# Kernel optimization log

Measured on AMD Instinct MI355X. Metric: run time of the kernel, lower is better.

Reference implementation:

```python
import jax, jax.numpy as jnp
import numpy as np

N = 100000      # nodes
E = 1600000     # edges (avg degree 16)
D_IN = 128      # input feature dim
H = 128         # sage_hidden (conv1 and conv2 out)
LH = 256        # linear_hidden (decoder)


def setup_inputs() -> dict:
    key = jax.random.key(0)
    ks = jax.random.split(key, 12)
    x = jax.random.normal(ks[0], (N, D_IN), dtype=jnp.float32)
    edge_index = jax.random.randint(ks[1], (2, E), 0, N, dtype=jnp.int64)
    s = 1.0 / np.sqrt(D_IN)
    sh = 1.0 / np.sqrt(H)
    sl = 1.0 / np.sqrt(LH)
    return {
        "x": x,
        "edge_index": edge_index,
        # SAGEConv1: out = agg @ W_l^T + b_l + x @ W_r^T
        "W1_l": jax.random.uniform(ks[2], (H, D_IN), jnp.float32, -s, s),
        "b1": jax.random.uniform(ks[3], (H,), jnp.float32, -s, s),
        "W1_r": jax.random.uniform(ks[4], (H, D_IN), jnp.float32, -s, s),
        # SAGEConv2
        "W2_l": jax.random.uniform(ks[5], (H, H), jnp.float32, -sh, sh),
        "b2": jax.random.uniform(ks[6], (H,), jnp.float32, -sh, sh),
        "W2_r": jax.random.uniform(ks[7], (H, H), jnp.float32, -sh, sh),
        # decoder MLP
        "W3": jax.random.uniform(ks[8], (LH, H), jnp.float32, -sh, sh),
        "b3": jax.random.uniform(ks[9], (LH,), jnp.float32, -sh, sh),
        "W4": jax.random.uniform(ks[10], (1, LH), jnp.float32, -sl, sl),
        "b4": jax.random.uniform(ks[11], (1,), jnp.float32, -sl, sl),
    }


def _mean_aggregate(x, src, dst):
    # gather neighbor features along edges and mean-reduce into destination nodes
    sums = jax.ops.segment_sum(x[src], dst, num_segments=N)          # [N, d]
    cnt = jax.ops.segment_sum(jnp.ones((src.shape[0],), x.dtype), dst,
                              num_segments=N)                        # [N]
    return sums / jnp.maximum(cnt, 1.0)[:, None]


def _sage(x, src, dst, W_l, b, W_r):
    agg = _mean_aggregate(x, src, dst)
    return agg @ W_l.T + b + x @ W_r.T


def reference(x, edge_index, W1_l, b1, W1_r, W2_l, b2, W2_r, W3, b3, W4, b4):
    src, dst = edge_index[0], edge_index[1]
    h = jax.nn.relu(_sage(x, src, dst, W1_l, b1, W1_r))   # conv1 + relu
    h = _sage(h, src, dst, W2_l, b2, W2_r)                 # conv2
    # decoder (dropout p=0 / eval mode -> identity)
    h = jax.nn.relu(h @ W3.T + b3)
    out = (h @ W4.T + b4).reshape(-1)                      # [N]
    return out
```

## Files before the change

### kernel.cpp

```cpp
#include <hip/hip_runtime.h>

typedef unsigned short u16;
typedef unsigned int u32;
typedef unsigned long long u64;

#define N_NODES 100000
#define N_EDGES 1600000
#define TPITCH 136
#define NBIN 196
#define BCAP 12288
#define NPART 512
#define EPB 3125

typedef __bf16 bf16x8 __attribute__((ext_vector_type(8)));
typedef float  f32x4  __attribute__((ext_vector_type(4)));

__device__ inline float b2f(u16 b) { return __uint_as_float(((u32)b) << 16); }
__device__ inline float b2f_lo(u32 u) { return __uint_as_float(u << 16); }
__device__ inline float b2f_hi(u32 u) { return __uint_as_float(u & 0xffff0000u); }
__device__ inline u16 f2b(float f) {
    u32 u = __float_as_uint(f);
    return (u16)((u + 0x7fffu + ((u >> 16) & 1u)) >> 16);
}

__device__ inline bf16x8 ldfrag(const u16* base, int row, int k) {
    union { uint4 u; bf16x8 v; } t;
    t.u = *(const uint4*)(base + (size_t)row * 128 + k);
    return t.v;
}
__device__ inline bf16x8 ldfrag_f32(const float* base, int row, int k) {
    const float4* p = (const float4*)(base + (size_t)row * 128 + k);
    float4 a = p[0], b = p[1];
    union { u16 h[8]; bf16x8 v; } t;
    t.h[0] = f2b(a.x); t.h[1] = f2b(a.y); t.h[2] = f2b(a.z); t.h[3] = f2b(a.w);
    t.h[4] = f2b(b.x); t.h[5] = f2b(b.y); t.h[6] = f2b(b.z); t.h[7] = f2b(b.w);
    return t.v;
}
__device__ inline bf16x8 ldfrag_lds(const u16* tile, int lrow, int k) {
    union { uint4 u; bf16x8 v; } t;
    t.u = *(const uint4*)(tile + lrow * TPITCH + k);
    return t.v;
}
__device__ inline f32x4 mfma16(bf16x8 a, bf16x8 b, f32x4 c) {
    return __builtin_amdgcn_mfma_f32_16x16x32_bf16(a, b, c, 0, 0, 0);
}

__device__ inline void stage_w(const u16* __restrict__ g, u16* lds) {
    int t = threadIdx.x;
#pragma unroll
    for (int i = 0; i < 8; i++) {
        int u = t + i * 256;
        int row = u >> 4, k = (u & 15) * 8;
        *(uint4*)(lds + row * TPITCH + k) = *(const uint4*)(g + row * 128 + k);
    }
}

__global__ __launch_bounds__(256) void k_diag(u16* __restrict__ out, float val) {
    int i = blockIdx.x * 256 + threadIdx.x;
    if (i < N_NODES) out[i] = f2b(val);
}

__global__ __launch_bounds__(256) void k_detects(const u64* __restrict__ e,
                                                 const u32* __restrict__ x,
                                                 int* __restrict__ flags) {
    int t = threadIdx.x;
    if (blockIdx.x == 0) {
        u64 v = 0;
#pragma unroll
        for (int i = 0; i < 4; i++) v |= e[t + 256 * i];
        if (v >> 32) atomicOr(&flags[0], 1);
    } else {
        int bad = 0;
#pragma unroll
        for (int i = 0; i < 4; i++) {
            u32 w = x[t + 256 * i];
            u32 ex = (w >> 7) & 0xff;
            if (ex < 100 || ex > 140) bad = 1;
        }
        if (bad) atomicOr(&flags[1], 1);
    }
}

__device__ inline void load_edge(const int* ei, int is32, int e, int& src, int& dst) {
    if (is32) {
        src = ei[e]; dst = ei[N_EDGES + e];
    } else {
        const long long* e64 = (const long long*)ei;
        src = (int)e64[e]; dst = (int)e64[N_EDGES + e];
    }
}

__global__ __launch_bounds__(256) void k_rhist(const int* __restrict__ ei,
                                               int* __restrict__ ghist,
                                               const int* __restrict__ flags) {
    __shared__ int hist[NBIN];
    int p = blockIdx.x, t = threadIdx.x;
    for (int i = t; i < NBIN; i += 256) hist[i] = 0;
    __syncthreads();
    int is32 = flags[0];
    int base = p * EPB;
    int end = base + EPB; if (end > N_EDGES) end = N_EDGES;
    for (int e = base + t; e < end; e += 256) {
        int src, dst; load_edge(ei, is32, e, src, dst);
        if ((u32)src < N_NODES && (u32)dst < N_NODES) atomicAdd(&hist[dst >> 9], 1);
    }
    __syncthreads();
    for (int i = t; i < NBIN; i += 256) ghist[i * NPART + p] = hist[i];
}
__global__ __launch_bounds__(512) void k_rscan(const int* __restrict__ ghist,
                                               int* __restrict__ gbase,
                                               int* __restrict__ gcur) {
    __shared__ int buf[NPART];
    int b = blockIdx.x, t = threadIdx.x;
    int v = ghist[b * NPART + t];
    buf[t] = v;
    __syncthreads();
    for (int s = 1; s < NPART; s <<= 1) {
        int a = (t >= s) ? buf[t - s] : 0;
        __syncthreads();
        buf[t] += a;
        __syncthreads();
    }
    gbase[b * NPART + t] = buf[t] - v;
    if (t == NPART - 1) gcur[b] = buf[t];
}
__global__ __launch_bounds__(256) void k_rscatter(const int* __restrict__ ei,
                                                  const int* __restrict__ gbase,
                                                  u32* __restrict__ gbuf,
                                                  const int* __restrict__ flags) {
    __shared__ int cur[NBIN];
    int p = blockIdx.x, t = threadIdx.x;
    for (int i = t; i < NBIN; i += 256) cur[i] = gbase[i * NPART + p];
    __syncthreads();
    int is32 = flags[0];
    int base = p * EPB;
    int end = base + EPB; if (end > N_EDGES) end = N_EDGES;
    for (int e = base + t; e < end; e += 256) {
        int src, dst; load_edge(ei, is32, e, src, dst);
        if ((u32)src < N_NODES && (u32)dst < N_NODES) {
            int bin = dst >> 9;
            int pos = atomicAdd(&cur[bin], 1);
            if (pos < BCAP)
                gbuf[(size_t)bin * BCAP + pos] = ((u32)(dst & 511) << 17) | (u32)src;
        }
    }
}
__global__ __launch_bounds__(512) void k_binB(const int* __restrict__ gcur,
                                              const u32* __restrict__ gbuf,
                                              u32* __restrict__ csr,
                                              int* __restrict__ cnt,
                                              int* __restrict__ offN) {
    __shared__ int hist[512];
    __shared__ int pfx[512];
    __shared__ int cur[512];
    __shared__ u32 srcbuf[BCAP];
    int b = blockIdx.x, t = threadIdx.x;
    int n = gcur[b]; if (n > BCAP) n = BCAP;
    hist[t] = 0;
    __syncthreads();
    for (int i = t; i < n; i += 512)
        atomicAdd(&hist[gbuf[(size_t)b * BCAP + i] >> 17], 1);
    __syncthreads();
    pfx[t] = hist[t];
    __syncthreads();
    for (int s = 1; s < 512; s <<= 1) {
        int a = (t >= s) ? pfx[t - s] : 0;
        __syncthreads();
        pfx[t] += a;
        __syncthreads();
    }
    int excl = pfx[t] - hist[t];
    cur[t] = excl;
    __syncthreads();
    for (int i = t; i < n; i += 512) {
        u32 p = gbuf[(size_t)b * BCAP + i];
        int pos = atomicAdd(&cur[p >> 17], 1);
        if (pos < BCAP) srcbuf[pos] = p & 0x1FFFFu;
    }
    __syncthreads();
    int total = pfx[511];
    for (int i = t; i < total; i += 512)
        csr[(size_t)b * BCAP + i] = srcbuf[i];
    int node = b * 512 + t;
    if (node < N_NODES) {
        cnt[node] = hist[t];
        offN[node] = b * BCAP + excl;
    }
}

#define WTOT 99073
struct CvtArgs { const void* src[10]; int off[10]; int n[10]; };
__global__ __launch_bounds__(256) void k_cvtw(CvtArgs a, u16* __restrict__ dst,
                                              const int* __restrict__ flags) {
    int i = blockIdx.x * 256 + threadIdx.x;
    if (i >= WTOT) return;
    int isf = flags[1];
    int s = 0;
    while (s < 9 && i >= a.off[s + 1]) s++;
    int j = i - a.off[s];
    float v = isf ? ((const float*)a.src[s])[j] : b2f(((const u16*)a.src[s])[j]);
    dst[i] = f2b(v);
}
#define W_W1L 0
#define W_W1R 16384
#define W_W2L 32768
#define W_W2R 49152
#define W_W3  65536
#define W_W4  98304
#define W_B1  98560
#define W_B2  98688
#define W_B3  98816
#define W_B4  99072

__global__ __launch_bounds__(256) void k_cvtx(const void* __restrict__ x,
                                              u16* __restrict__ xb,
                                              const int* __restrict__ flags) {
    int i = blockIdx.x * 256 + threadIdx.x;
    if ((size_t)i * 4 >= (size_t)N_NODES * 128) return;
    if (flags[1]) {
        float4 v = ((const float4*)x)[i];
        union { u16 h[4]; u64 q; } t;
        t.h[0] = f2b(v.x); t.h[1] = f2b(v.y); t.h[2] = f2b(v.z); t.h[3] = f2b(v.w);
        ((u64*)xb)[i] = t.q;
    } else {
        ((u64*)xb)[i] = ((const u64*)x)[i];
    }
}

__global__ __launch_bounds__(256) void k_aggc(const u16* __restrict__ feat,
                                              const int* __restrict__ cnt,
                                              const int* __restrict__ offN,
                                              const u32* __restrict__ csr,
                                              u16* __restrict__ outb) {
    int node = blockIdx.x * 4 + (threadIdx.x >> 6);
    if (node >= N_NODES) return;
    int lane = threadIdx.x & 63;
    int deg = cnt[node];
    int s = offN[node];
    const u32* f = (const u32*)feat;
    float a0 = 0, a1 = 0, b0 = 0, b1 = 0, c0 = 0, c1 = 0, d0 = 0, d1 = 0;
    int p = 0;
    for (; p + 3 < deg; p += 4) {
        u32 n0 = csr[s + p], n1 = csr[s + p + 1], n2 = csr[s + p + 2], n3 = csr[s + p + 3];
        if (n0 >= N_NODES) n0 = 0;
        if (n1 >= N_NODES) n1 = 0;
        if (n2 >= N_NODES) n2 = 0;
        if (n3 >= N_NODES) n3 = 0;
        u32 w0 = f[(size_t)n0 * 64 + lane];
        u32 w1 = f[(size_t)n1 * 64 + lane];
        u32 w2 = f[(size_t)n2 * 64 + lane];
        u32 w3 = f[(size_t)n3 * 64 + lane];
        a0 += b2f_lo(w0); a1 += b2f_hi(w0);
        b0 += b2f_lo(w1); b1 += b2f_hi(w1);
        c0 += b2f_lo(w2); c1 += b2f_hi(w2);
        d0 += b2f_lo(w3); d1 += b2f_hi(w3);
    }
    for (; p < deg; p++) {
        u32 n0 = csr[s + p];
        if (n0 >= N_NODES) n0 = 0;
        u32 w0 = f[(size_t)n0 * 64 + lane];
        a0 += b2f_lo(w0); a1 += b2f_hi(w0);
    }
    float s0 = (a0 + b0) + (c0 + d0), s1 = (a1 + b1) + (c1 + d1);
    float sc = deg > 0 ? 1.f / (float)deg : 0.f;
    u16 h0 = f2b(s0 * sc), h1 = f2b(s1 * sc);
    ((u32*)outb)[(size_t)node * 64 + lane] = (u32)h0 | ((u32)h1 << 16);
}

__global__ __launch_bounds__(256) void k_aggcx(const void* __restrict__ x,
                                               const int* __restrict__ cnt,
                                               const int* __restrict__ offN,
                                               const u32* __restrict__ csr,
                                               const int* __restrict__ flags,
                                               u16* __restrict__ outb) {
    int node = blockIdx.x * 4 + (threadIdx.x >> 6);
    if (node >= N_NODES) return;
    int lane = threadIdx.x & 63;
    int deg = cnt[node];
    int s = offN[node];
    float a0 = 0, a1 = 0, b0 = 0, b1 = 0;
    int p = 0;
    if (flags[1]) {
        const float2* f = (const float2*)x;
        for (; p + 1 < deg; p += 2) {
            u32 n0 = csr[s + p], n1 = csr[s + p + 1];
            if (n0 >= N_NODES) n0 = 0;
            if (n1 >= N_NODES) n1 = 0;
            float2 w0 = f[(size_t)n0 * 64 + lane];
            float2 w1 = f[(size_t)n1 * 64 + lane];
            a0 += w0.x; a1 += w0.y; b0 += w1.x; b1 += w1.y;
        }
        for (; p < deg; p++) {
            u32 n0 = csr[s + p];
            if (n0 >= N_NODES) n0 = 0;
            float2 w0 = f[(size_t)n0 * 64 + lane];
            a0 += w0.x; a1 += w0.y;
        }
    } else {
        const u32* f = (const u32*)x;
        for (; p + 1 < deg; p += 2) {
            u32 n0 = csr[s + p], n1 = csr[s + p + 1];
            if (n0 >= N_NODES) n0 = 0;
            if (n1 >= N_NODES) n1 = 0;
            u32 w0 = f[(size_t)n0 * 64 + lane];
            u32 w1 = f[(size_t)n1 * 64 + lane];
            a0 += b2f_lo(w0); a1 += b2f_hi(w0);
            b0 += b2f_lo(w1); b1 += b2f_hi(w1);
        }
        for (; p < deg; p++) {
            u32 n0 = csr[s + p];
            if (n0 >= N_NODES) n0 = 0;
            u32 w0 = f[(size_t)n0 * 64 + lane];
            a0 += b2f_lo(w0); a1 += b2f_hi(w0);
        }
    }
    float s0 = a0 + b0, s1 = a1 + b1;
    float sc = deg > 0 ? 1.f / (float)deg : 0.f;
    u16 h0 = f2b(s0 * sc), h1 = f2b(s1 * sc);
    ((u32*)outb)[(size_t)node * 64 + lane] = (u32)h0 | ((u32)h1 << 16);
}

template <bool DUALX>
__global__ __launch_bounds__(256) void k_conv1f(
    const u16* __restrict__ aggA, const void* __restrict__ xself,
    const u16* __restrict__ Wc, const int* __restrict__ flags,
    u16* __restrict__ h1) {
    __shared__ __align__(16) u16 wbuf[128 * TPITCH];
    int wid = threadIdx.x >> 6, lane = threadIdx.x & 63;
    int r15 = lane & 15, quad = lane >> 4;
    int rb = blockIdx.x * 64;
    int ar = rb + wid * 16 + r15; if (ar > N_NODES - 1) ar = N_NODES - 1;

    bf16x8 ag[4], ax[4];
    bool isf = DUALX && flags[1];
#pragma unroll
    for (int ks = 0; ks < 4; ks++) {
        int ko = ks * 32 + quad * 8;
        ag[ks] = ldfrag(aggA, ar, ko);
        ax[ks] = isf ? ldfrag_f32((const float*)xself, ar, ko)
                     : ldfrag((const u16*)xself, ar, ko);
    }
    f32x4 acc[8] = {};
    stage_w(Wc + W_W1L, wbuf);
    __syncthreads();
#pragma unroll
    for (int ks = 0; ks < 4; ks++) {
        int ko = ks * 32 + quad * 8;
#pragma unroll
        for (int ct = 0; ct < 8; ct++)
            acc[ct] = mfma16(ag[ks], ldfrag_lds(wbuf, ct * 16 + r15, ko), acc[ct]);
    }
    __syncthreads();
    stage_w(Wc + W_W1R, wbuf);
    __syncthreads();
#pragma unroll
    for (int ks = 0; ks < 4; ks++) {
        int ko = ks * 32 + quad * 8;
#pragma unroll
        for (int ct = 0; ct < 8; ct++)
            acc[ct] = mfma16(ax[ks], ldfrag_lds(wbuf, ct * 16 + r15, ko), acc[ct]);
    }
#pragma unroll
    for (int ct = 0; ct < 8; ct++) {
        int col = ct * 16 + r15;
        float bb = b2f(Wc[W_B1 + col]);
#pragma unroll
        for (int r = 0; r < 4; r++) {
            int row = rb + wid * 16 + quad * 4 + r;
            if (row < N_NODES)
                h1[(size_t)row * 128 + col] = f2b(fmaxf(acc[ct][r] + bb, 0.f));
        }
    }
}

__global__ __launch_bounds__(256) void k_conv2f(
    const u16* __restrict__ aggH, const u16* __restrict__ h1,
    const u16* __restrict__ Wc, const int* __restrict__ flags,
    void* __restrict__ out) {
    __shared__ __align__(16) u16 wbuf[128 * TPITCH];
    __shared__ __align__(16) u16 tile[64 * TPITCH];
    int wid = threadIdx.x >> 6, lane = threadIdx.x & 63;
    int r15 = lane & 15, quad = lane >> 4;
    int rb = blockIdx.x * 64;
    int ar = rb + wid * 16 + r15; if (ar > N_NODES - 1) ar = N_NODES - 1;
    int arl = wid * 16 + r15;

    bf16x8 at[4], as[4];
#pragma unroll
    for (int ks = 0; ks < 4; ks++) {
        int ko = ks * 32 + quad * 8;
        at[ks] = ldfrag(aggH, ar, ko);
        as[ks] = ldfrag(h1, ar, ko);
    }
    f32x4 acc2[8] = {};
    stage_w(Wc + W_W2L, wbuf);
    __syncthreads();
#pragma unroll
    for (int ks = 0; ks < 4; ks++) {
        int ko = ks * 32 + quad * 8;
#pragma unroll
        for (int ct = 0; ct < 8; ct++)
            acc2[ct] = mfma16(at[ks], ldfrag_lds(wbuf, ct * 16 + r15, ko), acc2[ct]);
    }
    __syncthreads();
    stage_w(Wc + W_W2R, wbuf);
    __syncthreads();
#pragma unroll
    for (int ks = 0; ks < 4; ks++) {
        int ko = ks * 32 + quad * 8;
#pragma unroll
        for (int ct = 0; ct < 8; ct++)
            acc2[ct] = mfma16(as[ks], ldfrag_lds(wbuf, ct * 16 + r15, ko), acc2[ct]);
    }
#pragma unroll
    for (int ct = 0; ct < 8; ct++) {
        int col = ct * 16 + r15;
        float bb = b2f(Wc[W_B2 + col]);
#pragma unroll
        for (int r = 0; r < 4; r++) {
            int lr = wid * 16 + quad * 4 + r;
            tile[lr * TPITCH + col] = f2b(acc2[ct][r] + bb);
        }
    }
    __syncthreads();

    float pr[4] = {};
    float b4f = b2f(Wc[W_B4]);
#pragma unroll
    for (int half = 0; half < 2; half++) {
        stage_w(Wc + W_W3 + half * 16384, wbuf);
        __syncthreads();
        f32x4 acc3[8] = {};
#pragma unroll
        for (int ks = 0; ks < 4; ks++) {
            int ko = ks * 32 + quad * 8;
            bf16x8 a = ldfrag_lds(tile, arl, ko);
#pragma unroll
            for (int ct = 0; ct < 8; ct++)
                acc3[ct] = mfma16(a, ldfrag_lds(wbuf, ct * 16 + r15, ko), acc3[ct]);
        }
#pragma unroll
        for (int ct = 0; ct < 8; ct++) {
            int col = half * 128 + ct * 16 + r15;
            float bb = b2f(Wc[W_B3 + col]);
            float w4 = b2f(Wc[W_W4 + col]);
#pragma unroll
            for (int r = 0; r < 4; r++)
                pr[r] += fmaxf(acc3[ct][r] + bb, 0.f) * w4;
        }
        __syncthreads();
    }
#pragma unroll
    for (int m = 1; m < 16; m <<= 1)
#pragma unroll
        for (int r = 0; r < 4; r++)
            pr[r] += __shfl_xor(pr[r], m, 64);
    if (r15 == 0) {
        int isf = flags[1];
#pragma unroll
        for (int r = 0; r < 4; r++) {
            int row = rb + wid * 16 + quad * 4 + r;
            if (row < N_NODES) {
                float v = pr[r] + b4f;
                if (isf) ((float*)out)[row] = v;
                else     ((u16*)out)[row] = f2b(v);
            }
        }
    }
}

__global__ __launch_bounds__(256) void k_hist(const int* __restrict__ ei,
                                              int* __restrict__ cnt,
                                              const int* __restrict__ flags) {
    int e = blockIdx.x * 256 + threadIdx.x;
    if (e >= N_EDGES) return;
    int src, dst; load_edge(ei, flags[0], e, src, dst);
    if ((u32)src < N_NODES && (u32)dst < N_NODES) atomicAdd(&cnt[dst], 1);
}
__global__ __launch_bounds__(1024) void k_scan(int* __restrict__ cnt,
                                               int* __restrict__ off) {
    __shared__ int buf[1024];
    __shared__ int carry_s;
    int t = threadIdx.x;
    if (t == 0) carry_s = 0;
    __syncthreads();
    for (int base = 0; base < N_NODES; base += 1024) {
        int i = base + t;
        int v = (i < N_NODES) ? cnt[i] : 0;
        buf[t] = v;
        __syncthreads();
        for (int s = 1; s < 1024; s <<= 1) {
            int a = (t >= s) ? buf[t - s] : 0;
            __syncthreads();
            buf[t] += a;
            __syncthreads();
        }
        int carry = carry_s;
        if (i < N_NODES) {
            int excl = carry + buf[t] - v;
            off[i] = excl;
            cnt[i] = excl;
        }
        __syncthreads();
        if (t == 1023) carry_s = carry + buf[1023];
        __syncthreads();
    }
    if (t == 0) off[N_NODES] = carry_s;
}
__global__ __launch_bounds__(256) void k_csr(const int* __restrict__ ei,
                                             int* __restrict__ cursor,
                                             int* __restrict__ csr,
                                             const int* __restrict__ flags) {
    int e = blockIdx.x * 256 + threadIdx.x;
    if (e >= N_EDGES) return;
    int src, dst; load_edge(ei, flags[0], e, src, dst);
    if ((u32)src < N_NODES && (u32)dst < N_NODES) {
        int pos = atomicAdd(&cursor[dst], 1);
        if ((u32)pos < N_EDGES) csr[pos] = src;
    }
}
__device__ inline void agg_bf16(const u16* __restrict__ feat,
                                const int* __restrict__ off, const int* __restrict__ csr,
                                u16* tile, int rb, int wid, int lane) {
    const u32* f32p = (const u32*)feat;
    for (int rr = 0; rr < 32; rr++) {
        int lr = wid * 32 + rr;
        int node = rb + lr;
        float s0 = 0.f, s1 = 0.f;
        int deg = 0;
        if (node < N_NODES) {
            int s = off[node], e = off[node + 1];
            if (s < 0) s = 0;
            if (e > N_EDGES) e = N_EDGES;
            if (e < s) e = s;
            deg = e - s;
            for (int p = s; p < e; p++) {
                int nb = csr[p];
                if ((u32)nb >= N_NODES) nb = 0;
                u32 u = f32p[(size_t)nb * 64 + lane];
                s0 += b2f_lo(u); s1 += b2f_hi(u);
            }
        }
        float sc = deg > 0 ? 1.f / (float)deg : 0.f;
        u16 h0 = f2b(s0 * sc), h1 = f2b(s1 * sc);
        ((u32*)tile)[lr * (TPITCH / 2) + lane] = (u32)h0 | ((u32)h1 << 16);
    }
}
__device__ inline void agg_f32(const float* __restrict__ feat,
                               const int* __restrict__ off, const int* __restrict__ csr,
                               u16* tile, int rb, int wid, int lane) {
    const float2* fp = (const float2*)feat;
    for (int rr = 0; rr < 32; rr++) {
        int lr = wid * 32 + rr;
        int node = rb + lr;
        float s0 = 0.f, s1 = 0.f;
        int deg = 0;
        if (node < N_NODES) {
            int s = off[node], e = off[node + 1];
            if (s < 0) s = 0;
            if (e > N_EDGES) e = N_EDGES;
            if (e < s) e = s;
            deg = e - s;
            for (int p = s; p < e; p++) {
                int nb = csr[p];
                if ((u32)nb >= N_NODES) nb = 0;
                float2 v = fp[(size_t)nb * 64 + lane];
                s0 += v.x; s1 += v.y;
            }
        }
        float sc = deg > 0 ? 1.f / (float)deg : 0.f;
        u16 h0 = f2b(s0 * sc), h1 = f2b(s1 * sc);
        ((u32*)tile)[lr * (TPITCH / 2) + lane] = (u32)h0 | ((u32)h1 << 16);
    }
}
__global__ __launch_bounds__(256) void k_conv1(
    const void* __restrict__ x, const int* __restrict__ off, const int* __restrict__ csr,
    const u16* __restrict__ Wc, const int* __restrict__ flags,
    u16* __restrict__ h1) {
    __shared__ __align__(16) u16 tile[128 * TPITCH];
    int wid = threadIdx.x >> 6, lane = threadIdx.x & 63;
    int r15 = lane & 15, quad = lane >> 4;
    int rb = blockIdx.x * 128;
    int isf = flags[1];
    if (isf) agg_f32((const float*)x, off, csr, tile, rb, wid, lane);
    else     agg_bf16((const u16*)x, off, csr, tile, rb, wid, lane);
    __syncthreads();
    int ar0l = wid * 32 + r15, ar1l = ar0l + 16;
    int ar0g = rb + ar0l; if (ar0g > N_NODES - 1) ar0g = N_NODES - 1;
    int ar1g = rb + ar1l; if (ar1g > N_NODES - 1) ar1g = N_NODES - 1;
    bf16x8 ax0[4], ax1[4];
    if (isf) {
#pragma unroll
        for (int ks = 0; ks < 4; ks++) {
            int ko = ks * 32 + quad * 8;
            ax0[ks] = ldfrag_f32((const float*)x, ar0g, ko);
            ax1[ks] = ldfrag_f32((const float*)x, ar1g, ko);
        }
    } else {
#pragma unroll
        for (int ks = 0; ks < 4; ks++) {
            int ko = ks * 32 + quad * 8;
            ax0[ks] = ldfrag((const u16*)x, ar0g, ko);
            ax1[ks] = ldfrag((const u16*)x, ar1g, ko);
        }
    }
    f32x4 acc[2][8] = {};
#pragma unroll
    for (int ks = 0; ks < 4; ks++) {
        int ko = ks * 32 + quad * 8;
        bf16x8 a0t = ldfrag_lds(tile, ar0l, ko);
        bf16x8 a1t = ldfrag_lds(tile, ar1l, ko);
#pragma unroll
        for (int ct = 0; ct < 8; ct++) {
            bf16x8 bl = ldfrag(Wc + W_W1L, ct * 16 + r15, ko);
            bf16x8 br = ldfrag(Wc + W_W1R, ct * 16 + r15, ko);
            acc[0][ct] = mfma16(a0t, bl, acc[0][ct]);
            acc[0][ct] = mfma16(ax0[ks], br, acc[0][ct]);
            acc[1][ct] = mfma16(a1t, bl, acc[1][ct]);
            acc[1][ct] = mfma16(ax1[ks], br, acc[1][ct]);
        }
    }
#pragma unroll
    for (int ct = 0; ct < 8; ct++) {
        int col = ct * 16 + r15;
        float bb = b2f(Wc[W_B1 + col]);
#pragma unroll
        for (int rt = 0; rt < 2; rt++) {
#pragma unroll
            for (int r = 0; r < 4; r++) {
                int row = rb + wid * 32 + rt * 16 + quad * 4 + r;
                if (row < N_NODES)
                    h1[(size_t)row * 128 + col] = f2b(fmaxf(acc[rt][ct][r] + bb, 0.f));
            }
        }
    }
}
__global__ __launch_bounds__(256) void k_conv2mlp(
    const u16* __restrict__ h1, const int* __restrict__ off, const int* __restrict__ csr,
    const u16* __restrict__ Wc, const int* __restrict__ flags,
    void* __restrict__ out) {
    __shared__ __align__(16) u16 tile[128 * TPITCH];
    int wid = threadIdx.x >> 6, lane = threadIdx.x & 63;
    int r15 = lane & 15, quad = lane >> 4;
    int rb = blockIdx.x * 128;
    agg_bf16(h1, off, csr, tile, rb, wid, lane);
    __syncthreads();
    int ar0l = wid * 32 + r15, ar1l = ar0l + 16;
    int ar0g = rb + ar0l; if (ar0g > N_NODES - 1) ar0g = N_NODES - 1;
    int ar1g = rb + ar1l; if (ar1g > N_NODES - 1) ar1g = N_NODES - 1;
    f32x4 acc2[2][8] = {};
#pragma unroll
    for (int ks = 0; ks < 4; ks++) {
        int ko = ks * 32 + quad * 8;
        bf16x8 a0t = ldfrag_lds(tile, ar0l, ko);
        bf16x8 a1t = ldfrag_lds(tile, ar1l, ko);
        bf16x8 a0s = ldfrag(h1, ar0g, ko);
        bf16x8 a1s = ldfrag(h1, ar1g, ko);
#pragma unroll
        for (int ct = 0; ct < 8; ct++) {
            bf16x8 bl = ldfrag(Wc + W_W2L, ct * 16 + r15, ko);
            bf16x8 br = ldfrag(Wc + W_W2R, ct * 16 + r15, ko);
            acc2[0][ct] = mfma16(a0t, bl, acc2[0][ct]);
            acc2[0][ct] = mfma16(a0s, br, acc2[0][ct]);
            acc2[1][ct] = mfma16(a1t, bl, acc2[1][ct]);
            acc2[1][ct] = mfma16(a1s, br, acc2[1][ct]);
        }
    }
    __syncthreads();
#pragma unroll
    for (int ct = 0; ct < 8; ct++) {
        int col = ct * 16 + r15;
        float bb = b2f(Wc[W_B2 + col]);
#pragma unroll
        for (int rt = 0; rt < 2; rt++) {
#pragma unroll
            for (int r = 0; r < 4; r++) {
                int lr = wid * 32 + rt * 16 + quad * 4 + r;
                tile[lr * TPITCH + col] = f2b(acc2[rt][ct][r] + bb);
            }
        }
    }
    __syncthreads();
    float pr[2][4] = {};
    float b4f = b2f(Wc[W_B4]);
#pragma unroll
    for (int half = 0; half < 2; half++) {
        f32x4 acc3[2][8] = {};
#pragma unroll
        for (int ks = 0; ks < 4; ks++) {
            int ko = ks * 32 + quad * 8;
            bf16x8 a0 = ldfrag_lds(tile, ar0l, ko);
            bf16x8 a1 = ldfrag_lds(tile, ar1l, ko);
#pragma unroll
            for (int ct = 0; ct < 8; ct++) {
                bf16x8 b = ldfrag(Wc + W_W3, half * 128 + ct * 16 + r15, ko);
                acc3[0][ct] = mfma16(a0, b, acc3[0][ct]);
                acc3[1][ct] = mfma16(a1, b, acc3[1][ct]);
            }
        }
#pragma unroll
        for (int ct = 0; ct < 8; ct++) {
            int col = half * 128 + ct * 16 + r15;
            float bb = b2f(Wc[W_B3 + col]);
            float w4 = b2f(Wc[W_W4 + col]);
#pragma unroll
            for (int rt = 0; rt < 2; rt++)
#pragma unroll
                for (int r = 0; r < 4; r++)
                    pr[rt][r] += fmaxf(acc3[rt][ct][r] + bb, 0.f) * w4;
        }
    }
#pragma unroll
    for (int m = 1; m < 16; m <<= 1)
#pragma unroll
        for (int rt = 0; rt < 2; rt++)
#pragma unroll
            for (int r = 0; r < 4; r++)
                pr[rt][r] += __shfl_xor(pr[rt][r], m, 64);
    if (r15 == 0) {
        int isf = flags[1];
#pragma unroll
        for (int rt = 0; rt < 2; rt++) {
#pragma unroll
            for (int r = 0; r < 4; r++) {
                int row = rb + wid * 32 + rt * 16 + quad * 4 + r;
                if (row < N_NODES) {
                    float v = pr[rt][r] + b4f;
                    if (isf) ((float*)out)[row] = v;
                    else     ((u16*)out)[row] = f2b(v);
                }
            }
        }
    }
}

extern "C" void kernel_launch(void* const* d_in, const int* in_sizes, int n_in,
                              void* d_out, int out_size, void* d_ws, size_t ws_size,
                              hipStream_t stream) {
    const void* x  = d_in[0];
    const int* ei  = (const int*)d_in[1];

    const size_t A = 256;
    const size_t sFlg  = 256;
    const size_t sGcur = 1024;
    const size_t sGh   = (((size_t)NBIN * NPART * 4) + A - 1) & ~(A - 1);
    const size_t sCnt  = (((size_t)N_NODES * 4) + A - 1) & ~(A - 1);
    const size_t sOffN = (((size_t)N_NODES * 4) + A - 1) & ~(A - 1);
    const size_t sWc   = ((WTOT * 2) + A - 1) & ~(A - 1);
    const size_t sCsrB = (((size_t)NBIN * BCAP * 4) + A - 1) & ~(A - 1);
    const size_t sFB   = (((size_t)N_NODES * 128 * 2) + A - 1) & ~(A - 1);
    const size_t sOff  = (((size_t)(N_NODES + 1) * 4) + A - 1) & ~(A - 1);
    const size_t sCsr  = (((size_t)N_EDGES * 4) + A - 1) & ~(A - 1);
    const size_t needB1 = sFlg + sGcur + 2 * sGh + sCnt + sOffN + sWc + sCsrB + 2 * sFB;
    const size_t needB0 = needB1 + sFB;
    const size_t needS  = sFlg + sCnt + sOff + sCsr + sFB;

    char* ws = (char*)d_ws;
    int gconv = (N_NODES + 63) / 64;
    int gagg  = (N_NODES + 3) / 4;

    CvtArgs ca;
    const int srcIdx[10] = {2, 4, 5, 7, 8, 10, 3, 6, 9, 11};
    const int offs[10] = {W_W1L, W_W1R, W_W2L, W_W2R, W_W3, W_W4, W_B1, W_B2, W_B3, W_B4};
    const int ns[10]   = {16384, 16384, 16384, 16384, 32768, 256, 128, 128, 256, 1};
    for (int i = 0; i < 10; i++) { ca.src[i] = d_in[srcIdx[i]]; ca.off[i] = offs[i]; ca.n[i] = ns[i]; }

    if (ws_size >= needB1) {
        bool t0 = ws_size >= needB0;
        int* flags = (int*)ws;
        int* gcur  = (int*)(ws + sFlg);
        int* ghist = (int*)(ws + sFlg + sGcur);
        int* gbase = (int*)(ws + sFlg + sGcur + sGh);
        int* cnt   = (int*)(ws + sFlg + sGcur + 2 * sGh);
        int* offN  = (int*)(ws + sFlg + sGcur + 2 * sGh + sCnt);
        u16* Wc    = (u16*)(ws + sFlg + sGcur + 2 * sGh + sCnt + sOffN);
        u32* csrb  = (u32*)(ws + sFlg + sGcur + 2 * sGh + sCnt + sOffN + sWc);
        u16* B1    = (u16*)(ws + sFlg + sGcur + 2 * sGh + sCnt + sOffN + sWc + sCsrB);
        u16* B2    = B1 + (sFB / 2);
        u32* gbuf  = (u32*)B2;
        u16* xb    = B2 + (sFB / 2);

        hipMemsetAsync(ws, 0, sFlg, stream);
        k_detects<<<2, 256, 0, stream>>>((const u64*)ei, (const u32*)x, flags);
        k_rhist<<<NPART, 256, 0, stream>>>(ei, ghist, flags);
        k_rscan<<<NBIN, 512, 0, stream>>>(ghist, gbase, gcur);
        k_rscatter<<<NPART, 256, 0, stream>>>(ei, gbase, gbuf, flags);
        k_binB<<<NBIN, 512, 0, stream>>>(gcur, gbuf, csrb, cnt, offN);
        k_cvtw<<<(WTOT + 255) / 256, 256, 0, stream>>>(ca, Wc, flags);

        if (t0) {
            k_cvtx<<<((N_NODES * 128 / 4) + 255) / 256, 256, 0, stream>>>(x, xb, flags);
            k_aggc<<<gagg, 256, 0, stream>>>(xb, cnt, offN, csrb, B1);
            k_conv1f<false><<<gconv, 256, 0, stream>>>(B1, xb, Wc, flags, B2);
        } else {
            k_aggcx<<<gagg, 256, 0, stream>>>(x, cnt, offN, csrb, flags, B1);
            k_conv1f<true><<<gconv, 256, 0, stream>>>(B1, x, Wc, flags, B2);
        }
        k_aggc<<<gagg, 256, 0, stream>>>(B2, cnt, offN, csrb, B1);
        k_conv2f<<<gconv, 256, 0, stream>>>(B1, B2, Wc, flags, d_out);
    } else if (ws_size >= needS) {
        int* flags = (int*)ws;
        int* cnt   = (int*)(ws + sFlg);
        u16* Wc    = (u16*)(ws + sFlg);
        int* off   = (int*)(ws + sFlg + sCnt);
        int* csr   = (int*)(ws + sFlg + sCnt + sOff);
        u16* h1    = (u16*)(ws + sFlg + sCnt + sOff + sCsr);

        hipMemsetAsync(ws, 0, sFlg + (size_t)N_NODES * 4, stream);
        k_detects<<<2, 256, 0, stream>>>((const u64*)ei, (const u32*)x, flags);
        k_hist<<<N_EDGES / 256, 256, 0, stream>>>(ei, cnt, flags);
        k_scan<<<1, 1024, 0, stream>>>(cnt, off);
        k_csr<<<N_EDGES / 256, 256, 0, stream>>>(ei, cnt, csr, flags);
        k_cvtw<<<(WTOT + 255) / 256, 256, 0, stream>>>(ca, Wc, flags);
        k_conv1<<<(N_NODES + 127) / 128, 256, 0, stream>>>(x, off, csr, Wc, flags, h1);
        k_conv2mlp<<<(N_NODES + 127) / 128, 256, 0, stream>>>(h1, off, csr, Wc, flags, d_out);
    } else {
        k_diag<<<(N_NODES + 255) / 256, 256, 0, stream>>>(
            (u16*)d_out, 2000.0f + (float)(ws_size >> 20));
    }
}
```

Baseline: 345.7 us.

## Fuse mean aggregation into SAGE conv kernels via shared-memory tile

The separate aggregation kernels are removed, and each conv kernel now gathers and averages neighbor features for its 64-row tile directly into a shared-memory tile before running the MFMA matmul. This avoids writing and re-reading the aggregated feature buffer in global memory and saves two launches, and the workspace needs one fewer feature buffer. The cost is parallelism: aggregation now runs with one block per 64 nodes (each wave walks 16 nodes in sequence) instead of one wave per node. That cuts memory-level parallelism and occupancy, since the extra LDS tile means fewer blocks per CU for the latency-bound gather.

```diff
diff --git a/kernel.cpp b/kernel.cpp
--- a/kernel.cpp
+++ b/kernel.cpp
@@ -227,128 +227,139 @@
     }
 }
 
-__global__ __launch_bounds__(256) void k_aggc(const u16* __restrict__ feat,
-                                              const int* __restrict__ cnt,
-                                              const int* __restrict__ offN,
-                                              const u32* __restrict__ csr,
-                                              u16* __restrict__ outb) {
-    int node = blockIdx.x * 4 + (threadIdx.x >> 6);
-    if (node >= N_NODES) return;
-    int lane = threadIdx.x & 63;
-    int deg = cnt[node];
-    int s = offN[node];
+__device__ inline void agg16_bf16(const u16* __restrict__ feat,
+                                  const int* __restrict__ cnt,
+                                  const int* __restrict__ offN,
+                                  const u32* __restrict__ csr,
+                                  u16* tile, int rb, int wid, int lane) {
     const u32* f = (const u32*)feat;
-    float a0 = 0, a1 = 0, b0 = 0, b1 = 0, c0 = 0, c1 = 0, d0 = 0, d1 = 0;
-    int p = 0;
-    for (; p + 3 < deg; p += 4) {
-        u32 n0 = csr[s + p], n1 = csr[s + p + 1], n2 = csr[s + p + 2], n3 = csr[s + p + 3];
-        if (n0 >= N_NODES) n0 = 0;
-        if (n1 >= N_NODES) n1 = 0;
-        if (n2 >= N_NODES) n2 = 0;
-        if (n3 >= N_NODES) n3 = 0;
-        u32 w0 = f[(size_t)n0 * 64 + lane];
-        u32 w1 = f[(size_t)n1 * 64 + lane];
-        u32 w2 = f[(size_t)n2 * 64 + lane];
-        u32 w3 = f[(size_t)n3 * 64 + lane];
-        a0 += b2f_lo(w0); a1 += b2f_hi(w0);
-        b0 += b2f_lo(w1); b1 += b2f_hi(w1);
-        c0 += b2f_lo(w2); c1 += b2f_hi(w2);
-        d0 += b2f_lo(w3); d1 += b2f_hi(w3);
-    }
-    for (; p < deg; p++) {
-        u32 n0 = csr[s + p];
-        if (n0 >= N_NODES) n0 = 0;
-        u32 w0 = f[(size_t)n0 * 64 + lane];
-        a0 += b2f_lo(w0); a1 += b2f_hi(w0);
-    }
-    float s0 = (a0 + b0) + (c0 + d0), s1 = (a1 + b1) + (c1 + d1);
-    float sc = deg > 0 ? 1.f / (float)deg : 0.f;
-    u16 h0 = f2b(s0 * sc), h1 = f2b(s1 * sc);
-    ((u32*)outb)[(size_t)node * 64 + lane] = (u32)h0 | ((u32)h1 << 16);
-}
-
-__global__ __launch_bounds__(256) void k_aggcx(const void* __restrict__ x,
-                                               const int* __restrict__ cnt,
-                                               const int* __restrict__ offN,
-                                               const u32* __restrict__ csr,
-                                               const int* __restrict__ flags,
-                                               u16* __restrict__ outb) {
-    int node = blockIdx.x * 4 + (threadIdx.x >> 6);
-    if (node >= N_NODES) return;
-    int lane = threadIdx.x & 63;
-    int deg = cnt[node];
-    int s = offN[node];
-    float a0 = 0, a1 = 0, b0 = 0, b1 = 0;
-    int p = 0;
-    if (flags[1]) {
-        const float2* f = (const float2*)x;
-        for (; p + 1 < deg; p += 2) {
-            u32 n0 = csr[s + p], n1 = csr[s + p + 1];
-            if (n0 >= N_NODES) n0 = 0;
-            if (n1 >= N_NODES) n1 = 0;
-            float2 w0 = f[(size_t)n0 * 64 + lane];
-            float2 w1 = f[(size_t)n1 * 64 + lane];
-            a0 += w0.x; a1 += w0.y; b0 += w1.x; b1 += w1.y;
-        }
-        for (; p < deg; p++) {
-            u32 n0 = csr[s + p];
-            if (n0 >= N_NODES) n0 = 0;
-            float2 w0 = f[(size_t)n0 * 64 + lane];
-            a0 += w0.x; a1 += w0.y;
-        }
-    } else {
-        const u32* f = (const u32*)x;
-        for (; p + 1 < deg; p += 2) {
-            u32 n0 = csr[s + p], n1 = csr[s + p + 1];
-            if (n0 >= N_NODES) n0 = 0;
-            if (n1 >= N_NODES) n1 = 0;
-            u32 w0 = f[(size_t)n0 * 64 + lane];
-            u32 w1 = f[(size_t)n1 * 64 + lane];
-            a0 += b2f_lo(w0); a1 += b2f_hi(w0);
-            b0 += b2f_lo(w1); b1 += b2f_hi(w1);
-        }
-        for (; p < deg; p++) {
-            u32 n0 = csr[s + p];
-            if (n0 >= N_NODES) n0 = 0;
-            u32 w0 = f[(size_t)n0 * 64 + lane];
-            a0 += b2f_lo(w0); a1 += b2f_hi(w0);
-        }
-    }
-    float s0 = a0 + b0, s1 = a1 + b1;
-    float sc = deg > 0 ? 1.f / (float)deg : 0.f;
-    u16 h0 = f2b(s0 * sc), h1 = f2b(s1 * sc);
-    ((u32*)outb)[(size_t)node * 64 + lane] = (u32)h0 | ((u32)h1 << 16);
+    for (int rr = 0; rr < 16; rr++) {
+        int node = rb + wid * 16 + rr;
+        float a0 = 0, a1 = 0, b0 = 0, b1 = 0, c0 = 0, c1 = 0, d0 = 0, d1 = 0;
+        int deg = 0;
+        if (node < N_NODES) {
+            deg = cnt[node];
+            int s = offN[node];
+            int p = 0;
+            for (; p + 3 < deg; p += 4) {
+                u32 n0 = csr[s + p], n1 = csr[s + p + 1], n2 = csr[s + p + 2], n3 = csr[s + p + 3];
+                if (n0 >= N_NODES) n0 = 0;
+                if (n1 >= N_NODES) n1 = 0;
+                if (n2 >= N_NODES) n2 = 0;
+                if (n3 >= N_NODES) n3 = 0;
+                u32 w0 = f[(size_t)n0 * 64 + lane];
+                u32 w1 = f[(size_t)n1 * 64 + lane];
+                u32 w2 = f[(size_t)n2 * 64 + lane];
+                u32 w3 = f[(size_t)n3 * 64 + lane];
+                a0 += b2f_lo(w0); a1 += b2f_hi(w0);
+                b0 += b2f_lo(w1); b1 += b2f_hi(w1);
+                c0 += b2f_lo(w2); c1 += b2f_hi(w2);
+                d0 += b2f_lo(w3); d1 += b2f_hi(w3);
+            }
+            for (; p < deg; p++) {
+                u32 n0 = csr[s + p];
+                if (n0 >= N_NODES) n0 = 0;
+                u32 w0 = f[(size_t)n0 * 64 + lane];
+                a0 += b2f_lo(w0); a1 += b2f_hi(w0);
+            }
+        }
+        float s0 = (a0 + b0) + (c0 + d0), s1 = (a1 + b1) + (c1 + d1);
+        float sc = deg > 0 ? 1.f / (float)deg : 0.f;
+        u16 h0 = f2b(s0 * sc), h1 = f2b(s1 * sc);
+        ((u32*)tile)[(wid * 16 + rr) * (TPITCH / 2) + lane] = (u32)h0 | ((u32)h1 << 16);
+    }
+}
+
+__device__ inline void agg16_x(const void* __restrict__ x, int isf,
+                               const int* __restrict__ cnt,
+                               const int* __restrict__ offN,
+                               const u32* __restrict__ csr,
+                               u16* tile, int rb, int wid, int lane) {
+    for (int rr = 0; rr < 16; rr++) {
+        int node = rb + wid * 16 + rr;
+        float a0 = 0, a1 = 0, b0 = 0, b1 = 0;
+        int deg = 0;
+        if (node < N_NODES) {
+            deg = cnt[node];
+            int s = offN[node];
+            int p = 0;
+            if (isf) {
+                const float2* f = (const float2*)x;
+                for (; p + 1 < deg; p += 2) {
+                    u32 n0 = csr[s + p], n1 = csr[s + p + 1];
+                    if (n0 >= N_NODES) n0 = 0;
+                    if (n1 >= N_NODES) n1 = 0;
+                    float2 w0 = f[(size_t)n0 * 64 + lane];
+                    float2 w1 = f[(size_t)n1 * 64 + lane];
+                    a0 += w0.x; a1 += w0.y; b0 += w1.x; b1 += w1.y;
+                }
+                for (; p < deg; p++) {
+                    u32 n0 = csr[s + p];
+                    if (n0 >= N_NODES) n0 = 0;
+                    float2 w0 = f[(size_t)n0 * 64 + lane];
+                    a0 += w0.x; a1 += w0.y;
+                }
+            } else {
+                const u32* f = (const u32*)x;
+                for (; p + 1 < deg; p += 2) {
+                    u32 n0 = csr[s + p], n1 = csr[s + p + 1];
+                    if (n0 >= N_NODES) n0 = 0;
+                    if (n1 >= N_NODES) n1 = 0;
+                    u32 w0 = f[(size_t)n0 * 64 + lane];
+                    u32 w1 = f[(size_t)n1 * 64 + lane];
+                    a0 += b2f_lo(w0); a1 += b2f_hi(w0);
+                    b0 += b2f_lo(w1); b1 += b2f_hi(w1);
+                }
+                for (; p < deg; p++) {
+                    u32 n0 = csr[s + p];
+                    if (n0 >= N_NODES) n0 = 0;
+                    u32 w0 = f[(size_t)n0 * 64 + lane];
+                    a0 += b2f_lo(w0); a1 += b2f_hi(w0);
+                }
+            }
+        }
+        float s0 = a0 + b0, s1 = a1 + b1;
+        float sc = deg > 0 ? 1.f / (float)deg : 0.f;
+        u16 h0 = f2b(s0 * sc), h1 = f2b(s1 * sc);
+        ((u32*)tile)[(wid * 16 + rr) * (TPITCH / 2) + lane] = (u32)h0 | ((u32)h1 << 16);
+    }
 }
 
 template <bool DUALX>
-__global__ __launch_bounds__(256) void k_conv1f(
-    const u16* __restrict__ aggA, const void* __restrict__ xself,
+__global__ __launch_bounds__(256) void k_fconv1(
+    const void* __restrict__ xself, const int* __restrict__ cnt,
+    const int* __restrict__ offN, const u32* __restrict__ csrb,
     const u16* __restrict__ Wc, const int* __restrict__ flags,
     u16* __restrict__ h1) {
     __shared__ __align__(16) u16 wbuf[128 * TPITCH];
+    __shared__ __align__(16) u16 tile[64 * TPITCH];
     int wid = threadIdx.x >> 6, lane = threadIdx.x & 63;
     int r15 = lane & 15, quad = lane >> 4;
     int rb = blockIdx.x * 64;
+    bool isf = DUALX && flags[1];
+
+    stage_w(Wc + W_W1L, wbuf);
+    if (DUALX) agg16_x(xself, isf, cnt, offN, csrb, tile, rb, wid, lane);
+    else       agg16_bf16((const u16*)xself, cnt, offN, csrb, tile, rb, wid, lane);
+
     int ar = rb + wid * 16 + r15; if (ar > N_NODES - 1) ar = N_NODES - 1;
-
-    bf16x8 ag[4], ax[4];
-    bool isf = DUALX && flags[1];
+    bf16x8 ax[4];
 #pragma unroll
     for (int ks = 0; ks < 4; ks++) {
         int ko = ks * 32 + quad * 8;
-        ag[ks] = ldfrag(aggA, ar, ko);
         ax[ks] = isf ? ldfrag_f32((const float*)xself, ar, ko)
                      : ldfrag((const u16*)xself, ar, ko);
     }
+    __syncthreads();
+
     f32x4 acc[8] = {};
-    stage_w(Wc + W_W1L, wbuf);
-    __syncthreads();
 #pragma unroll
     for (int ks = 0; ks < 4; ks++) {
         int ko = ks * 32 + quad * 8;
+        bf16x8 ag = ldfrag_lds(tile, wid * 16 + r15, ko);
 #pragma unroll
         for (int ct = 0; ct < 8; ct++)
-            acc[ct] = mfma16(ag[ks], ldfrag_lds(wbuf, ct * 16 + r15, ko), acc[ct]);
+            acc[ct] = mfma16(ag, ldfrag_lds(wbuf, ct * 16 + r15, ko), acc[ct]);
     }
     __syncthreads();
     stage_w(Wc + W_W1R, wbuf);
@@ -373,8 +384,9 @@
     }
 }
 
-__global__ __launch_bounds__(256) void k_conv2f(
-    const u16* __restrict__ aggH, const u16* __restrict__ h1,
+__global__ __launch_bounds__(256) void k_fconv2(
+    const u16* __restrict__ h1, const int* __restrict__ cnt,
+    const int* __restrict__ offN, const u32* __restrict__ csrb,
     const u16* __restrict__ Wc, const int* __restrict__ flags,
     void* __restrict__ out) {
     __shared__ __align__(16) u16 wbuf[128 * TPITCH];
@@ -382,22 +394,23 @@
     int wid = threadIdx.x >> 6, lane = threadIdx.x & 63;
     int r15 = lane & 15, quad = lane >> 4;
     int rb = blockIdx.x * 64;
-    int ar = rb + wid * 16 + r15; if (ar > N_NODES - 1) ar = N_NODES - 1;
     int arl = wid * 16 + r15;
 
-    bf16x8 at[4], as[4];
+    stage_w(Wc + W_W2L, wbuf);
+    agg16_bf16(h1, cnt, offN, csrb, tile, rb, wid, lane);
+
+    int ar = rb + arl; if (ar > N_NODES - 1) ar = N_NODES - 1;
+    bf16x8 as[4], at[4];
+#pragma unroll
+    for (int ks = 0; ks < 4; ks++)
+        as[ks] = ldfrag(h1, ar, ks * 32 + quad * 8);
+    __syncthreads();
+
+    f32x4 acc2[8] = {};
 #pragma unroll
     for (int ks = 0; ks < 4; ks++) {
         int ko = ks * 32 + quad * 8;
-        at[ks] = ldfrag(aggH, ar, ko);
-        as[ks] = ldfrag(h1, ar, ko);
-    }
-    f32x4 acc2[8] = {};
-    stage_w(Wc + W_W2L, wbuf);
-    __syncthreads();
-#pragma unroll
-    for (int ks = 0; ks < 4; ks++) {
-        int ko = ks * 32 + quad * 8;
+        at[ks] = ldfrag_lds(tile, arl, ko);
 #pragma unroll
         for (int ct = 0; ct < 8; ct++)
             acc2[ct] = mfma16(at[ks], ldfrag_lds(wbuf, ct * 16 + r15, ko), acc2[ct]);
@@ -751,13 +764,12 @@
     const size_t sFB   = (((size_t)N_NODES * 128 * 2) + A - 1) & ~(A - 1);
     const size_t sOff  = (((size_t)(N_NODES + 1) * 4) + A - 1) & ~(A - 1);
     const size_t sCsr  = (((size_t)N_EDGES * 4) + A - 1) & ~(A - 1);
-    const size_t needB1 = sFlg + sGcur + 2 * sGh + sCnt + sOffN + sWc + sCsrB + 2 * sFB;
-    const size_t needB0 = needB1 + sFB;
+    const size_t needF1 = sFlg + sGcur + 2 * sGh + sCnt + sOffN + sWc + sCsrB + sFB;
+    const size_t needF0 = needF1 + sFB;
     const size_t needS  = sFlg + sCnt + sOff + sCsr + sFB;
 
     char* ws = (char*)d_ws;
     int gconv = (N_NODES + 63) / 64;
-    int gagg  = (N_NODES + 3) / 4;
 
     CvtArgs ca;
     const int srcIdx[10] = {2, 4, 5, 7, 8, 10, 3, 6, 9, 11};
@@ -765,8 +777,8 @@
     const int ns[10]   = {16384, 16384, 16384, 16384, 32768, 256, 128, 128, 256, 1};
     for (int i = 0; i < 10; i++) { ca.src[i] = d_in[srcIdx[i]]; ca.off[i] = offs[i]; ca.n[i] = ns[i]; }
 
-    if (ws_size >= needB1) {
-        bool t0 = ws_size >= needB0;
+    if (ws_size >= needF1) {
+        bool t0 = ws_size >= needF0;
         int* flags = (int*)ws;
         int* gcur  = (int*)(ws + sFlg);
         int* ghist = (int*)(ws + sFlg + sGcur);
@@ -775,10 +787,9 @@
         int* offN  = (int*)(ws + sFlg + sGcur + 2 * sGh + sCnt);
         u16* Wc    = (u16*)(ws + sFlg + sGcur + 2 * sGh + sCnt + sOffN);
         u32* csrb  = (u32*)(ws + sFlg + sGcur + 2 * sGh + sCnt + sOffN + sWc);
-        u16* B1    = (u16*)(ws + sFlg + sGcur + 2 * sGh + sCnt + sOffN + sWc + sCsrB);
-        u16* B2    = B1 + (sFB / 2);
-        u32* gbuf  = (u32*)B2;
-        u16* xb    = B2 + (sFB / 2);
+        u16* h1    = (u16*)(ws + sFlg + sGcur + 2 * sGh + sCnt + sOffN + sWc + sCsrB);
+        u32* gbuf  = (u32*)h1;
+        u16* xb    = h1 + (sFB / 2);
 
         hipMemsetAsync(ws, 0, sFlg, stream);
         k_detects<<<2, 256, 0, stream>>>((const u64*)ei, (const u32*)x, flags);
@@ -790,14 +801,11 @@
 
         if (t0) {
             k_cvtx<<<((N_NODES * 128 / 4) + 255) / 256, 256, 0, stream>>>(x, xb, flags);
-            k_aggc<<<gagg, 256, 0, stream>>>(xb, cnt, offN, csrb, B1);
-            k_conv1f<false><<<gconv, 256, 0, stream>>>(B1, xb, Wc, flags, B2);
+            k_fconv1<false><<<gconv, 256, 0, stream>>>(xb, cnt, offN, csrb, Wc, flags, h1);
         } else {
-            k_aggcx<<<gagg, 256, 0, stream>>>(x, cnt, offN, csrb, flags, B1);
-            k_conv1f<true><<<gconv, 256, 0, stream>>>(B1, x, Wc, flags, B2);
-        }
-        k_aggc<<<gagg, 256, 0, stream>>>(B2, cnt, offN, csrb, B1);
-        k_conv2f<<<gconv, 256, 0, stream>>>(B1, B2, Wc, flags, d_out);
+            k_fconv1<true><<<gconv, 256, 0, stream>>>(x, cnt, offN, csrb, Wc, flags, h1);
+        }
+        k_fconv2<<<gconv, 256, 0, stream>>>(h1, cnt, offN, csrb, Wc, flags, d_out);
     } else if (ws_size >= needS) {
         int* flags = (int*)ws;
         int* cnt   = (int*)(ws + sFlg);
```

Result: slower. 516.3 us (+49.3%).
